# Performance work log

Hardware: AMD Instinct MI355X
Metric: run time of the kernel (lower is better)

Reference implementation:

```python
import jax, jax.numpy as jnp
import numpy as np

FP8_E4M3_MAX = 448.0  # torch.finfo(torch.float8_e4m3fn).max
TOKENS, D_IN, D_OUT = 8192, 4096, 4096


def setup_inputs() -> dict:
    key = jax.random.key(0)
    kx, kw, kb = jax.random.split(key, 3)
    x = jax.random.normal(kx, (TOKENS, D_IN), dtype=jnp.float32)
    # frozen bf16-like master weight, quantized to fp8 with per-tensor scale (as in __init__)
    w = jax.random.normal(kw, (D_OUT, D_IN), dtype=jnp.float32) * 0.02
    amax = jnp.abs(w).max()
    weight_scale = jnp.maximum(amax / FP8_E4M3_MAX, 1e-12).reshape(1)
    weight_fp8 = (w / weight_scale).astype(jnp.float8_e4m3fn)
    bias = jax.random.normal(kb, (D_OUT,), dtype=jnp.float32) * 0.01
    return {"x": x, "weight_fp8": weight_fp8, "weight_scale": weight_scale, "bias": bias}


def reference(x, weight_fp8, weight_scale, bias):
    # dequantize fp8 weight to activation dtype, scalar per-tensor scale
    w = weight_fp8.astype(x.dtype) * weight_scale.astype(x.dtype)  # [D_OUT, D_IN]
    return x @ w.T + bias  # [TOKENS, D_OUT]
```

## Files before the change

### kernel.cpp

```cpp
#include <hip/hip_runtime.h>


#define TILE 128
#define BKK  64
#define BK32 32
#define BM256 256
#define BN256 256

typedef __attribute__((ext_vector_type(8))) __bf16 bfrag8;
typedef __attribute__((ext_vector_type(4))) float  f32x4;
typedef __attribute__((ext_vector_type(8))) short  s8v;

#define GLOBAL_AS(p) ((const __attribute__((address_space(1))) void*)(p))
#define LDS_AS(p)    ((__attribute__((address_space(3))) void*)(p))

__device__ inline unsigned short f2bf(float f) {
    union { float f; unsigned u; } v; v.f = f;
    unsigned r = v.u + 0x7FFFu + ((v.u >> 16) & 1u);
    return (unsigned short)(r >> 16);
}
__device__ inline float bf2f(unsigned short u) {
    union { unsigned u; float f; } v; v.u = ((unsigned)u) << 16;
    return v.f;
}

__device__ inline int detect_w_f32(const void* w) {
    const unsigned short* u = (const unsigned short*)w;
    unsigned nz = 0;
#pragma unroll
    for (int i = 0; i < 64; ++i) nz |= u[2 * i];
    return nz == 0 ? 1 : 0;
}

__global__ void FP8FL_cvt_x(const float* __restrict__ x, short* __restrict__ xb, long n) {
    long i = ((long)blockIdx.x * blockDim.x + threadIdx.x) * 8;
    if (i >= n) return;
    float4 a = *(const float4*)(x + i);
    float4 b = *(const float4*)(x + i + 4);
    s8v r;
    r[0] = (short)f2bf(a.x); r[1] = (short)f2bf(a.y);
    r[2] = (short)f2bf(a.z); r[3] = (short)f2bf(a.w);
    r[4] = (short)f2bf(b.x); r[5] = (short)f2bf(b.y);
    r[6] = (short)f2bf(b.z); r[7] = (short)f2bf(b.w);
    *(s8v*)(xb + i) = r;
}

__global__ void FP8FL_cvt_w(const void* __restrict__ w, short* __restrict__ wb,
                            const float* __restrict__ scale_p, long n) {
    __shared__ int sdt;
    if (threadIdx.x == 0) sdt = detect_w_f32(w);
    __syncthreads();
    long i = ((long)blockIdx.x * blockDim.x + threadIdx.x) * 8;
    if (i >= n) return;
    const float s = scale_p[0];
    s8v r;
    if (sdt) {
        const float* wf = (const float*)w;
        float4 a = *(const float4*)(wf + i);
        float4 b = *(const float4*)(wf + i + 4);
        r[0] = (short)f2bf(a.x * s); r[1] = (short)f2bf(a.y * s);
        r[2] = (short)f2bf(a.z * s); r[3] = (short)f2bf(a.w * s);
        r[4] = (short)f2bf(b.x * s); r[5] = (short)f2bf(b.y * s);
        r[6] = (short)f2bf(b.z * s); r[7] = (short)f2bf(b.w * s);
    } else {
        const unsigned short* wu = (const unsigned short*)w;
        s8v v = *(const s8v*)(wu + i);
#pragma unroll
        for (int j = 0; j < 8; ++j)
            r[j] = (short)f2bf(bf2f((unsigned short)v[j]) * s);
    }
    *(s8v*)(wb + i) = r;
}

__device__ inline void stage_tile3(const short* __restrict__ A, const short* __restrict__ B,
                                   long row0, long col0, int K, int kc,
                                   char* __restrict__ lds, int s, int wid, int lane) {
    char* Asl = lds + s * 32768;
    char* Bsl = Asl + 16384;
#pragma unroll
    for (int i = 0; i < 2; ++i) {
        int pc = i * 512 + wid * 64 + lane;
        int r  = pc >> 2;
        int j  = (pc & 3) ^ ((r >> 1) & 3);
        const short* ga = A + (size_t)(row0 + r) * K + kc + j * 8;
        const short* gb = B + (size_t)(col0 + r) * K + kc + j * 8;
        char* da = Asl + (i * 512 + wid * 64) * 16;
        char* db = Bsl + (i * 512 + wid * 64) * 16;
        __builtin_amdgcn_global_load_lds(GLOBAL_AS(ga), LDS_AS(da), 16, 0, 0);
        __builtin_amdgcn_global_load_lds(GLOBAL_AS(gb), LDS_AS(db), 16, 0, 0);
    }
}

__global__ __launch_bounds__(512, 2)
void FP8FL_gemm256(const short* __restrict__ A, const short* __restrict__ B,
                   const float* __restrict__ bias, float* __restrict__ C,
                   int M, int N, int K) {
    __shared__ char lds[3 * 32768];

    const int tid  = threadIdx.x;
    const int lane = tid & 63;
    const int wid  = tid >> 6;

    const int nwg = gridDim.x;
    const int bid = blockIdx.x;
    const int wg  = (nwg % 8 == 0) ? (bid % 8) * (nwg / 8) + (bid / 8) : bid;

    const int tiles_n = N / BN256;
    const long row0 = (long)(wg / tiles_n) * BM256;
    const long col0 = (long)(wg % tiles_n) * BN256;

    const int wm = wid >> 2, wn = wid & 3;
    const int rl = lane & 15, g = lane >> 4;

    f32x4 acc[8][4];
#pragma unroll
    for (int m = 0; m < 8; ++m)
#pragma unroll
        for (int n = 0; n < 4; ++n) acc[m][n] = (f32x4){0.f, 0.f, 0.f, 0.f};

    const int NT = K / BK32;

    stage_tile3(A, B, row0, col0, K, 0,    lds, 0, wid, lane);
    stage_tile3(A, B, row0, col0, K, BK32, lds, 1, wid, lane);
    asm volatile("s_waitcnt vmcnt(4)" ::: "memory");
    __builtin_amdgcn_s_barrier();
    __builtin_amdgcn_sched_barrier(0);

    int scur = 0, snxt = 2;
    for (int t = 0; t < NT; ++t) {
        if (t + 2 < NT)
            stage_tile3(A, B, row0, col0, K, (t + 2) * BK32, lds, snxt, wid, lane);

        const char* Asl = lds + scur * 32768;
        const char* Bsl = Asl + 16384;
        bfrag8 af[8], bf[4];
#pragma unroll
        for (int m = 0; m < 8; ++m) {
            int r  = wm * 128 + m * 16 + rl;
            int sl = g ^ ((r >> 1) & 3);
            af[m] = *(const bfrag8*)(Asl + (r * 4 + sl) * 16);
        }
#pragma unroll
        for (int n = 0; n < 4; ++n) {
            int r  = wn * 64 + n * 16 + rl;
            int sl = g ^ ((r >> 1) & 3);
            bf[n] = *(const bfrag8*)(Bsl + (r * 4 + sl) * 16);
        }

        __builtin_amdgcn_s_setprio(1);
#pragma unroll
        for (int m = 0; m < 8; ++m)
#pragma unroll
            for (int n = 0; n < 4; ++n)
                acc[m][n] = __builtin_amdgcn_mfma_f32_16x16x32_bf16(af[m], bf[n], acc[m][n], 0, 0, 0);
        __builtin_amdgcn_s_setprio(0);

        if (t + 2 < NT) asm volatile("s_waitcnt vmcnt(4)" ::: "memory");
        else            asm volatile("s_waitcnt vmcnt(0)" ::: "memory");
        __builtin_amdgcn_s_barrier();
        __builtin_amdgcn_sched_barrier(0);

        scur = (scur == 2) ? 0 : scur + 1;
        snxt = (snxt == 2) ? 0 : snxt + 1;
    }

    float bv[4];
#pragma unroll
    for (int n = 0; n < 4; ++n) bv[n] = bias[col0 + wn * 64 + n * 16 + rl];
#pragma unroll
    for (int m = 0; m < 8; ++m) {
#pragma unroll
        for (int jj = 0; jj < 4; ++jj) {
            long r = row0 + wm * 128 + m * 16 + g * 4 + jj;
            float* cp = C + r * (long)N + col0 + wn * 64 + rl;
#pragma unroll
            for (int n = 0; n < 4; ++n) cp[n * 16] = acc[m][n][jj] + bv[n];
        }
    }
}

__global__ void FP8FL_gemm(const short* __restrict__ A, const short* __restrict__ B,
                           const float* __restrict__ bias, float* __restrict__ C,
                           int M, int N, int K) {
    __shared__ short As[TILE * BKK];
    __shared__ short Bs[TILE * BKK];

    const int tid  = threadIdx.x;
    const int lane = tid & 63;
    const int wid  = tid >> 6;

    const int nwg = gridDim.x;
    const int bid = blockIdx.x;
    const int wg  = (nwg % 8 == 0) ? (bid % 8) * (nwg / 8) + (bid / 8) : bid;

    const int tiles_n = N / TILE;
    const long row0 = (long)(wg / tiles_n) * TILE;
    const long col0 = (long)(wg % tiles_n) * TILE;

    const int wm = wid >> 1, wn = wid & 1;

    f32x4 acc[4][4];
#pragma unroll
    for (int i = 0; i < 4; ++i)
#pragma unroll
        for (int j = 0; j < 4; ++j) acc[i][j] = (f32x4){0.f, 0.f, 0.f, 0.f};

    const int rl = lane & 15;
    const int g  = lane >> 4;

    for (int k0 = 0; k0 < K; k0 += BKK) {
        __syncthreads();
#pragma unroll
        for (int i = 0; i < 4; ++i) {
            int c  = i * 256 + tid;
            int r  = c >> 3;
            int ls = c & 7;
            const short* ga = A + ((size_t)(row0 + r) * K + k0 + ls * 8);
            const short* gb = B + ((size_t)(col0 + r) * K + k0 + ls * 8);
            int ldsoff = (i * 256 + wid * 64) * 16;
            __builtin_amdgcn_global_load_lds(GLOBAL_AS(ga), LDS_AS((char*)As + ldsoff), 16, 0, 0);
            __builtin_amdgcn_global_load_lds(GLOBAL_AS(gb), LDS_AS((char*)Bs + ldsoff), 16, 0, 0);
        }
        __syncthreads();

#pragma unroll
        for (int kk = 0; kk < 2; ++kk) {
            bfrag8 af[4], bfr[4];
            const int lsk = kk * 4 + g;
#pragma unroll
            for (int m = 0; m < 4; ++m) {
                int r  = wm * 64 + m * 16 + rl;
                af[m] = *(const bfrag8*)&As[r * 64 + lsk * 8];
            }
#pragma unroll
            for (int n = 0; n < 4; ++n) {
                int r  = wn * 64 + n * 16 + rl;
                bfr[n] = *(const bfrag8*)&Bs[r * 64 + lsk * 8];
            }
#pragma unroll
            for (int m = 0; m < 4; ++m)
#pragma unroll
                for (int n = 0; n < 4; ++n)
                    acc[m][n] = __builtin_amdgcn_mfma_f32_16x16x32_bf16(af[m], bfr[n], acc[m][n], 0, 0, 0);
        }
    }

    float bv[4];
#pragma unroll
    for (int n = 0; n < 4; ++n) bv[n] = bias[col0 + wn * 64 + n * 16 + rl];
#pragma unroll
    for (int m = 0; m < 4; ++m) {
#pragma unroll
        for (int j = 0; j < 4; ++j) {
            long r = row0 + wm * 64 + m * 16 + g * 4 + j;
            float* cp = C + r * (long)N + col0 + wn * 64 + rl;
#pragma unroll
            for (int n = 0; n < 4; ++n) cp[n * 16] = acc[m][n][j] + bv[n];
        }
    }
}

__global__ void FP8FL_gemm_fused(const float* __restrict__ X, const void* __restrict__ W,
                                 const float* __restrict__ scale_p,
                                 const float* __restrict__ bias, float* __restrict__ C,
                                 int M, int N, int K) {
    __shared__ short As[TILE * BKK];
    __shared__ short Bs[TILE * BKK];
    __shared__ int sdt;

    const int tid  = threadIdx.x;
    const int lane = tid & 63;
    const int wid  = tid >> 6;

    if (tid == 0) sdt = detect_w_f32(W);
    __syncthreads();
    const int wdt = sdt;
    const float s = scale_p[0];

    const int nwg = gridDim.x;
    const int bid = blockIdx.x;
    const int wg  = (nwg % 8 == 0) ? (bid % 8) * (nwg / 8) + (bid / 8) : bid;

    const int tiles_n = N / TILE;
    const long row0 = (long)(wg / tiles_n) * TILE;
    const long col0 = (long)(wg % tiles_n) * TILE;

    const int wm = wid >> 1, wn = wid & 1;

    f32x4 acc[4][4];
#pragma unroll
    for (int i = 0; i < 4; ++i)
#pragma unroll
        for (int j = 0; j < 4; ++j) acc[i][j] = (f32x4){0.f, 0.f, 0.f, 0.f};

    const int rl = lane & 15;
    const int g  = lane >> 4;

    for (int k0 = 0; k0 < K; k0 += BKK) {
        s8v va[4], vb[4];
#pragma unroll
        for (int i = 0; i < 4; ++i) {
            int c  = i * 256 + tid;
            int r  = c >> 3;
            int ls = c & 7;
            {
                const float* xp = X + ((size_t)(row0 + r) * K + k0 + ls * 8);
                float4 a = *(const float4*)xp;
                float4 b = *(const float4*)(xp + 4);
                s8v t;
                t[0] = (short)f2bf(a.x); t[1] = (short)f2bf(a.y);
                t[2] = (short)f2bf(a.z); t[3] = (short)f2bf(a.w);
                t[4] = (short)f2bf(b.x); t[5] = (short)f2bf(b.y);
                t[6] = (short)f2bf(b.z); t[7] = (short)f2bf(b.w);
                va[i] = t;
            }
            {
                size_t off = (size_t)(col0 + r) * K + k0 + ls * 8;
                s8v t;
                if (wdt) {
                    const float* wp = (const float*)W + off;
                    float4 a = *(const float4*)wp;
                    float4 b = *(const float4*)(wp + 4);
                    t[0] = (short)f2bf(a.x * s); t[1] = (short)f2bf(a.y * s);
                    t[2] = (short)f2bf(a.z * s); t[3] = (short)f2bf(a.w * s);
                    t[4] = (short)f2bf(b.x * s); t[5] = (short)f2bf(b.y * s);
                    t[6] = (short)f2bf(b.z * s); t[7] = (short)f2bf(b.w * s);
                } else {
                    const unsigned short* wp = (const unsigned short*)W + off;
                    s8v v = *(const s8v*)wp;
#pragma unroll
                    for (int j = 0; j < 8; ++j)
                        t[j] = (short)f2bf(bf2f((unsigned short)v[j]) * s);
                }
                vb[i] = t;
            }
        }
        __syncthreads();
#pragma unroll
        for (int i = 0; i < 4; ++i) {
            int c = i * 256 + tid;
            *(s8v*)((char*)As + (size_t)c * 16) = va[i];
            *(s8v*)((char*)Bs + (size_t)c * 16) = vb[i];
        }
        __syncthreads();

#pragma unroll
        for (int kk = 0; kk < 2; ++kk) {
            bfrag8 af[4], bfr[4];
            const int lsk = kk * 4 + g;
#pragma unroll
            for (int m = 0; m < 4; ++m) {
                int r  = wm * 64 + m * 16 + rl;
                af[m] = *(const bfrag8*)&As[r * 64 + lsk * 8];
            }
#pragma unroll
            for (int n = 0; n < 4; ++n) {
                int r  = wn * 64 + n * 16 + rl;
                bfr[n] = *(const bfrag8*)&Bs[r * 64 + lsk * 8];
            }
#pragma unroll
            for (int m = 0; m < 4; ++m)
#pragma unroll
                for (int n = 0; n < 4; ++n)
                    acc[m][n] = __builtin_amdgcn_mfma_f32_16x16x32_bf16(af[m], bfr[n], acc[m][n], 0, 0, 0);
        }
    }

    float bv[4];
#pragma unroll
    for (int n = 0; n < 4; ++n) bv[n] = bias[col0 + wn * 64 + n * 16 + rl];
#pragma unroll
    for (int m = 0; m < 4; ++m) {
#pragma unroll
        for (int j = 0; j < 4; ++j) {
            long r = row0 + wm * 64 + m * 16 + g * 4 + j;
            float* cp = C + r * (long)N + col0 + wn * 64 + rl;
#pragma unroll
            for (int n = 0; n < 4; ++n) cp[n * 16] = acc[m][n][j] + bv[n];
        }
    }
}

__global__ void FP8FL_naive(const float* __restrict__ x, const void* __restrict__ w,
                            const float* __restrict__ scale_p, const float* __restrict__ bias,
                            float* __restrict__ out, int M, int N, int K) {
    __shared__ int sdt;
    if (threadIdx.x == 0) sdt = detect_w_f32(w);
    __syncthreads();
    long o = (long)blockIdx.x * blockDim.x + threadIdx.x;
    if (o >= (long)M * N) return;
    int m = (int)(o / N), n = (int)(o % N);
    const float* xr = x + (size_t)m * K;
    float acc = 0.f;
    if (sdt) {
        const float* wr = (const float*)w + (size_t)n * K;
        for (int k = 0; k < K; ++k) acc += xr[k] * wr[k];
    } else {
        const unsigned short* wr = (const unsigned short*)w + (size_t)n * K;
        for (int k = 0; k < K; ++k) acc += xr[k] * bf2f(wr[k]);
    }
    out[o] = acc * scale_p[0] + bias[n];
}

extern "C" void kernel_launch(void* const* d_in, const int* in_sizes, int n_in,
                              void* d_out, int out_size, void* d_ws, size_t ws_size,
                              hipStream_t stream) {
    const float* x     = (const float*)d_in[0];
    const void*  w     = d_in[1];
    const float* scale = (const float*)d_in[2];
    const float* bias  = (const float*)d_in[3];
    float*       out   = (float*)d_out;

    const int N = in_sizes[3];
    const int K = in_sizes[1] / N;
    const int M = in_sizes[0] / K;

    const size_t need = (size_t)M * K * 2 + (size_t)N * K * 2;
    const bool ws_ok   = ws_size >= need;
    const bool dims256 = (M % BM256 == 0) && (N % BN256 == 0) && (K % BKK == 0) && (K / BK32 >= 4);
    const bool dims128 = (M % TILE == 0) && (N % TILE == 0) && (K % BKK == 0);

    if (ws_ok && (dims256 || dims128)) {
        short* xb = (short*)d_ws;
        short* wb = (short*)((char*)d_ws + (size_t)M * K * 2);
        long nx = (long)M * K;
        long nw = (long)N * K;
        FP8FL_cvt_x<<<(int)((nx / 8 + 255) / 256), 256, 0, stream>>>(x, xb, nx);
        FP8FL_cvt_w<<<(int)((nw / 8 + 255) / 256), 256, 0, stream>>>(w, wb, scale, nw);
        if (dims256) {
            int grid = (M / BM256) * (N / BN256);
            FP8FL_gemm256<<<grid, 512, 0, stream>>>(xb, wb, bias, out, M, N, K);
        } else {
            int grid = (M / TILE) * (N / TILE);
            FP8FL_gemm<<<grid, 256, 0, stream>>>(xb, wb, bias, out, M, N, K);
        }
    } else if (dims128) {
        int grid = (M / TILE) * (N / TILE);
        FP8FL_gemm_fused<<<grid, 256, 0, stream>>>(x, w, scale, bias, out, M, N, K);
    } else {
        long total = (long)M * N;
        FP8FL_naive<<<(int)((total + 255) / 256), 256, 0, stream>>>(x, w, scale, bias, out, M, N, K);
    }
}
```

Measured before the change: 291.5 us.

## Split GEMM K-step into two half phases interleaving LDS reads, prefetch and MFMA

Each K iteration is split into two halves. Each half loads its A fragments from LDS, issues half of the next tile's global-to-LDS prefetch, then runs 16 MFMAs, with extra barriers between the phases. The aim is to spread global load issue across the compute and cut register pressure by holding only half the A fragments at a time. In exchange it adds several workgroup barriers per iteration, which can add synchronisation stalls.

```diff
diff --git a/kernel.cpp b/kernel.cpp
--- a/kernel.cpp
+++ b/kernel.cpp
@@ -72,20 +72,22 @@
     *(s8v*)(wb + i) = r;
 }
 
-__device__ inline void stage_tile3(const short* __restrict__ A, const short* __restrict__ B,
+__device__ inline void stage_half3(const short* __restrict__ A, const short* __restrict__ B,
                                    long row0, long col0, int K, int kc,
-                                   char* __restrict__ lds, int s, int wid, int lane) {
+                                   char* __restrict__ lds, int s, int h,
+                                   int wid, int lane) {
     char* Asl = lds + s * 32768;
     char* Bsl = Asl + 16384;
 #pragma unroll
-    for (int i = 0; i < 2; ++i) {
-        int pc = i * 512 + wid * 64 + lane;
+    for (int i = 0; i < 1; ++i) {}
+    {
+        int pc = (h ? 512 : 0) + wid * 64 + lane;
         int r  = pc >> 2;
         int j  = (pc & 3) ^ ((r >> 1) & 3);
         const short* ga = A + (size_t)(row0 + r) * K + kc + j * 8;
         const short* gb = B + (size_t)(col0 + r) * K + kc + j * 8;
-        char* da = Asl + (i * 512 + wid * 64) * 16;
-        char* db = Bsl + (i * 512 + wid * 64) * 16;
+        char* da = Asl + ((h ? 512 : 0) + wid * 64) * 16;
+        char* db = Bsl + ((h ? 512 : 0) + wid * 64) * 16;
         __builtin_amdgcn_global_load_lds(GLOBAL_AS(ga), LDS_AS(da), 16, 0, 0);
         __builtin_amdgcn_global_load_lds(GLOBAL_AS(gb), LDS_AS(db), 16, 0, 0);
     }
@@ -120,25 +122,27 @@
 
     const int NT = K / BK32;
 
-    stage_tile3(A, B, row0, col0, K, 0,    lds, 0, wid, lane);
-    stage_tile3(A, B, row0, col0, K, BK32, lds, 1, wid, lane);
+    stage_half3(A, B, row0, col0, K, 0,    lds, 0, 0, wid, lane);
+    stage_half3(A, B, row0, col0, K, 0,    lds, 0, 1, wid, lane);
+    stage_half3(A, B, row0, col0, K, BK32, lds, 1, 0, wid, lane);
+    stage_half3(A, B, row0, col0, K, BK32, lds, 1, 1, wid, lane);
     asm volatile("s_waitcnt vmcnt(4)" ::: "memory");
     __builtin_amdgcn_s_barrier();
     __builtin_amdgcn_sched_barrier(0);
 
     int scur = 0, snxt = 2;
     for (int t = 0; t < NT; ++t) {
-        if (t + 2 < NT)
-            stage_tile3(A, B, row0, col0, K, (t + 2) * BK32, lds, snxt, wid, lane);
-
         const char* Asl = lds + scur * 32768;
         const char* Bsl = Asl + 16384;
-        bfrag8 af[8], bf[4];
-#pragma unroll
-        for (int m = 0; m < 8; ++m) {
+        const bool pf = (t + 2 < NT);
+        const int  kc2 = (t + 2) * BK32;
+
+        bfrag8 a0[4], bf[4], a1[4];
+#pragma unroll
+        for (int m = 0; m < 4; ++m) {
             int r  = wm * 128 + m * 16 + rl;
             int sl = g ^ ((r >> 1) & 3);
-            af[m] = *(const bfrag8*)(Asl + (r * 4 + sl) * 16);
+            a0[m] = *(const bfrag8*)(Asl + (r * 4 + sl) * 16);
         }
 #pragma unroll
         for (int n = 0; n < 4; ++n) {
@@ -146,17 +150,42 @@
             int sl = g ^ ((r >> 1) & 3);
             bf[n] = *(const bfrag8*)(Bsl + (r * 4 + sl) * 16);
         }
-
+        if (pf) stage_half3(A, B, row0, col0, K, kc2, lds, snxt, 0, wid, lane);
+
+        __builtin_amdgcn_s_barrier();
+        asm volatile("s_waitcnt lgkmcnt(0)" ::: "memory");
+        __builtin_amdgcn_sched_barrier(0);
         __builtin_amdgcn_s_setprio(1);
 #pragma unroll
-        for (int m = 0; m < 8; ++m)
+        for (int m = 0; m < 4; ++m)
 #pragma unroll
             for (int n = 0; n < 4; ++n)
-                acc[m][n] = __builtin_amdgcn_mfma_f32_16x16x32_bf16(af[m], bf[n], acc[m][n], 0, 0, 0);
+                acc[m][n] = __builtin_amdgcn_mfma_f32_16x16x32_bf16(a0[m], bf[n], acc[m][n], 0, 0, 0);
         __builtin_amdgcn_s_setprio(0);
-
-        if (t + 2 < NT) asm volatile("s_waitcnt vmcnt(4)" ::: "memory");
-        else            asm volatile("s_waitcnt vmcnt(0)" ::: "memory");
+        __builtin_amdgcn_s_barrier();
+        __builtin_amdgcn_sched_barrier(0);
+
+#pragma unroll
+        for (int m = 0; m < 4; ++m) {
+            int r  = wm * 128 + (m + 4) * 16 + rl;
+            int sl = g ^ ((r >> 1) & 3);
+            a1[m] = *(const bfrag8*)(Asl + (r * 4 + sl) * 16);
+        }
+        if (pf) stage_half3(A, B, row0, col0, K, kc2, lds, snxt, 1, wid, lane);
+
+        __builtin_amdgcn_s_barrier();
+        asm volatile("s_waitcnt lgkmcnt(0)" ::: "memory");
+        __builtin_amdgcn_sched_barrier(0);
+        __builtin_amdgcn_s_setprio(1);
+#pragma unroll
+        for (int m = 0; m < 4; ++m)
+#pragma unroll
+            for (int n = 0; n < 4; ++n)
+                acc[m + 4][n] = __builtin_amdgcn_mfma_f32_16x16x32_bf16(a1[m], bf[n], acc[m + 4][n], 0, 0, 0);
+        __builtin_amdgcn_s_setprio(0);
+
+        if (pf) asm volatile("s_waitcnt vmcnt(4)" ::: "memory");
+        else    asm volatile("s_waitcnt vmcnt(0)" ::: "memory");
         __builtin_amdgcn_s_barrier();
         __builtin_amdgcn_sched_barrier(0);
 
```

Result: slower. 300.7 us (+3.1%).

## Shrink GEMM tile to 256x128 with double-buffered LDS and higher occupancy

Applied to the files above, without the earlier changes.

Replaces the 256x256 bf16 GEMM tile with a 256x128 tile, halving per-wave accumulators from 8x4 to 4x4 MFMA fragments. Launch bounds now request 4 workgroups per CU instead of 2. The LDS pipeline drops from triple buffering with explicit vmcnt waits to double buffering with plain __syncthreads. The aim is more resident waves and more tiles to spread across CUs, at the cost of less operand reuse per tile and more global traffic for A. The simpler synchronisation may also expose load latency that the earlier three-stage pipeline hid.

```diff
diff --git a/kernel.cpp b/kernel.cpp
--- a/kernel.cpp
+++ b/kernel.cpp
@@ -4,8 +4,8 @@
 #define TILE 128
 #define BKK  64
 #define BK32 32
-#define BM256 256
-#define BN256 256
+#define BM   256
+#define BN   128
 
 typedef __attribute__((ext_vector_type(8))) __bf16 bfrag8;
 typedef __attribute__((ext_vector_type(4))) float  f32x4;
@@ -72,10 +72,10 @@
     *(s8v*)(wb + i) = r;
 }
 
-__device__ inline void stage_tile3(const short* __restrict__ A, const short* __restrict__ B,
-                                   long row0, long col0, int K, int kc,
-                                   char* __restrict__ lds, int s, int wid, int lane) {
-    char* Asl = lds + s * 32768;
+__device__ inline void stage_tile(const short* __restrict__ A, const short* __restrict__ B,
+                                  long row0, long col0, int K, int kc,
+                                  char* __restrict__ lds, int d, int wid, int lane) {
+    char* Asl = lds + d * 24576;
     char* Bsl = Asl + 16384;
 #pragma unroll
     for (int i = 0; i < 2; ++i) {
@@ -83,19 +83,24 @@
         int r  = pc >> 2;
         int j  = (pc & 3) ^ ((r >> 1) & 3);
         const short* ga = A + (size_t)(row0 + r) * K + kc + j * 8;
+        char* da = Asl + (i * 512 + wid * 64) * 16;
+        __builtin_amdgcn_global_load_lds(GLOBAL_AS(ga), LDS_AS(da), 16, 0, 0);
+    }
+    {
+        int pc = wid * 64 + lane;
+        int r  = pc >> 2;
+        int j  = (pc & 3) ^ ((r >> 1) & 3);
         const short* gb = B + (size_t)(col0 + r) * K + kc + j * 8;
-        char* da = Asl + (i * 512 + wid * 64) * 16;
-        char* db = Bsl + (i * 512 + wid * 64) * 16;
-        __builtin_amdgcn_global_load_lds(GLOBAL_AS(ga), LDS_AS(da), 16, 0, 0);
+        char* db = Bsl + (wid * 64) * 16;
         __builtin_amdgcn_global_load_lds(GLOBAL_AS(gb), LDS_AS(db), 16, 0, 0);
     }
 }
 
-__global__ __launch_bounds__(512, 2)
-void FP8FL_gemm256(const short* __restrict__ A, const short* __restrict__ B,
-                   const float* __restrict__ bias, float* __restrict__ C,
-                   int M, int N, int K) {
-    __shared__ char lds[3 * 32768];
+__global__ __launch_bounds__(512, 4)
+void FP8FL_gemm256x128(const short* __restrict__ A, const short* __restrict__ B,
+                       const float* __restrict__ bias, float* __restrict__ C,
+                       int M, int N, int K) {
+    __shared__ char lds[2 * 24576];
 
     const int tid  = threadIdx.x;
     const int lane = tid & 63;
@@ -105,38 +110,35 @@
     const int bid = blockIdx.x;
     const int wg  = (nwg % 8 == 0) ? (bid % 8) * (nwg / 8) + (bid / 8) : bid;
 
-    const int tiles_n = N / BN256;
-    const long row0 = (long)(wg / tiles_n) * BM256;
-    const long col0 = (long)(wg % tiles_n) * BN256;
-
-    const int wm = wid >> 2, wn = wid & 3;
+    const int tiles_n = N / BN;
+    const long row0 = (long)(wg / tiles_n) * BM;
+    const long col0 = (long)(wg % tiles_n) * BN;
+
+    const int wm = wid >> 1, wn = wid & 1;
     const int rl = lane & 15, g = lane >> 4;
 
-    f32x4 acc[8][4];
-#pragma unroll
-    for (int m = 0; m < 8; ++m)
+    f32x4 acc[4][4];
+#pragma unroll
+    for (int m = 0; m < 4; ++m)
 #pragma unroll
         for (int n = 0; n < 4; ++n) acc[m][n] = (f32x4){0.f, 0.f, 0.f, 0.f};
 
     const int NT = K / BK32;
 
-    stage_tile3(A, B, row0, col0, K, 0,    lds, 0, wid, lane);
-    stage_tile3(A, B, row0, col0, K, BK32, lds, 1, wid, lane);
-    asm volatile("s_waitcnt vmcnt(4)" ::: "memory");
-    __builtin_amdgcn_s_barrier();
-    __builtin_amdgcn_sched_barrier(0);
-
-    int scur = 0, snxt = 2;
+    stage_tile(A, B, row0, col0, K, 0, lds, 0, wid, lane);
+    __syncthreads();
+
     for (int t = 0; t < NT; ++t) {
-        if (t + 2 < NT)
-            stage_tile3(A, B, row0, col0, K, (t + 2) * BK32, lds, snxt, wid, lane);
-
-        const char* Asl = lds + scur * 32768;
+        const int d = t & 1;
+        if (t + 1 < NT)
+            stage_tile(A, B, row0, col0, K, (t + 1) * BK32, lds, d ^ 1, wid, lane);
+
+        const char* Asl = lds + d * 24576;
         const char* Bsl = Asl + 16384;
-        bfrag8 af[8], bf[4];
-#pragma unroll
-        for (int m = 0; m < 8; ++m) {
-            int r  = wm * 128 + m * 16 + rl;
+        bfrag8 af[4], bf[4];
+#pragma unroll
+        for (int m = 0; m < 4; ++m) {
+            int r  = wm * 64 + m * 16 + rl;
             int sl = g ^ ((r >> 1) & 3);
             af[m] = *(const bfrag8*)(Asl + (r * 4 + sl) * 16);
         }
@@ -149,29 +151,23 @@
 
         __builtin_amdgcn_s_setprio(1);
 #pragma unroll
-        for (int m = 0; m < 8; ++m)
+        for (int m = 0; m < 4; ++m)
 #pragma unroll
             for (int n = 0; n < 4; ++n)
                 acc[m][n] = __builtin_amdgcn_mfma_f32_16x16x32_bf16(af[m], bf[n], acc[m][n], 0, 0, 0);
         __builtin_amdgcn_s_setprio(0);
 
-        if (t + 2 < NT) asm volatile("s_waitcnt vmcnt(4)" ::: "memory");
-        else            asm volatile("s_waitcnt vmcnt(0)" ::: "memory");
-        __builtin_amdgcn_s_barrier();
-        __builtin_amdgcn_sched_barrier(0);
-
-        scur = (scur == 2) ? 0 : scur + 1;
-        snxt = (snxt == 2) ? 0 : snxt + 1;
+        __syncthreads();
     }
 
     float bv[4];
 #pragma unroll
     for (int n = 0; n < 4; ++n) bv[n] = bias[col0 + wn * 64 + n * 16 + rl];
 #pragma unroll
-    for (int m = 0; m < 8; ++m) {
+    for (int m = 0; m < 4; ++m) {
 #pragma unroll
         for (int jj = 0; jj < 4; ++jj) {
-            long r = row0 + wm * 128 + m * 16 + g * 4 + jj;
+            long r = row0 + wm * 64 + m * 16 + g * 4 + jj;
             float* cp = C + r * (long)N + col0 + wn * 64 + rl;
 #pragma unroll
             for (int n = 0; n < 4; ++n) cp[n * 16] = acc[m][n][jj] + bv[n];
@@ -417,19 +413,19 @@
 
     const size_t need = (size_t)M * K * 2 + (size_t)N * K * 2;
     const bool ws_ok   = ws_size >= need;
-    const bool dims256 = (M % BM256 == 0) && (N % BN256 == 0) && (K % BKK == 0) && (K / BK32 >= 4);
+    const bool dimsBig = (M % BM == 0) && (N % BN == 0) && (K % BK32 == 0) && (K / BK32 >= 2);
     const bool dims128 = (M % TILE == 0) && (N % TILE == 0) && (K % BKK == 0);
 
-    if (ws_ok && (dims256 || dims128)) {
+    if (ws_ok && (dimsBig || dims128)) {
         short* xb = (short*)d_ws;
         short* wb = (short*)((char*)d_ws + (size_t)M * K * 2);
         long nx = (long)M * K;
         long nw = (long)N * K;
         FP8FL_cvt_x<<<(int)((nx / 8 + 255) / 256), 256, 0, stream>>>(x, xb, nx);
         FP8FL_cvt_w<<<(int)((nw / 8 + 255) / 256), 256, 0, stream>>>(w, wb, scale, nw);
-        if (dims256) {
-            int grid = (M / BM256) * (N / BN256);
-            FP8FL_gemm256<<<grid, 512, 0, stream>>>(xb, wb, bias, out, M, N, K);
+        if (dimsBig) {
+            int grid = (M / BM) * (N / BN);
+            FP8FL_gemm256x128<<<grid, 512, 0, stream>>>(xb, wb, bias, out, M, N, K);
         } else {
             int grid = (M / TILE) * (N / TILE);
             FP8FL_gemm<<<grid, 256, 0, stream>>>(xb, wb, bias, out, M, N, K);
```

After: 317.2 us. 8.8% more time.

## Deepen LDS ring to four stages and prefetch next A fragments into registers

Applied to the files above, without the earlier changes.

The bf16 GEMM main loop moves from a 3-slot to a 4-slot LDS ring, prefetching three K-tiles ahead. It is unrolled by two so the A fragments for the next tile are read from LDS into a second register buffer while the current tile's MFMAs run. The goal is to hide global-load latency and LDS read latency behind MFMA work. In exchange it uses 128 KB of LDS per block instead of 96 KB and needs more VGPRs for the extra fragment buffer. The sched_barrier calls that constrained instruction scheduling are also removed.

```diff
diff --git a/kernel.cpp b/kernel.cpp
--- a/kernel.cpp
+++ b/kernel.cpp
@@ -72,7 +72,7 @@
     *(s8v*)(wb + i) = r;
 }
 
-__device__ inline void stage_tile3(const short* __restrict__ A, const short* __restrict__ B,
+__device__ inline void stage_tile4(const short* __restrict__ A, const short* __restrict__ B,
                                    long row0, long col0, int K, int kc,
                                    char* __restrict__ lds, int s, int wid, int lane) {
     char* Asl = lds + s * 32768;
@@ -91,11 +91,43 @@
     }
 }
 
+#define RD_A(dst, sbase)                                                    \
+    {                                                                       \
+        _Pragma("unroll")                                                   \
+        for (int m = 0; m < 8; ++m) {                                       \
+            int r  = wm * 128 + m * 16 + rl;                                \
+            int sl = g ^ ((r >> 1) & 3);                                    \
+            dst[m] = *(const bfrag8*)((sbase) + (r * 4 + sl) * 16);         \
+        }                                                                   \
+    }
+
+#define RD_B(dst, sbase)                                                    \
+    {                                                                       \
+        _Pragma("unroll")                                                   \
+        for (int n = 0; n < 4; ++n) {                                       \
+            int r  = wn * 64 + n * 16 + rl;                                 \
+            int sl = g ^ ((r >> 1) & 3);                                    \
+            dst[n] = *(const bfrag8*)((sbase) + 16384 + (r * 4 + sl) * 16); \
+        }                                                                   \
+    }
+
+#define MM(fa, bb)                                                          \
+    {                                                                       \
+        __builtin_amdgcn_s_setprio(1);                                      \
+        _Pragma("unroll")                                                   \
+        for (int m = 0; m < 8; ++m)                                         \
+            _Pragma("unroll")                                               \
+            for (int n = 0; n < 4; ++n)                                     \
+                acc[m][n] = __builtin_amdgcn_mfma_f32_16x16x32_bf16(        \
+                    fa[m], bb[n], acc[m][n], 0, 0, 0);                      \
+        __builtin_amdgcn_s_setprio(0);                                      \
+    }
+
 __global__ __launch_bounds__(512, 2)
 void FP8FL_gemm256(const short* __restrict__ A, const short* __restrict__ B,
                    const float* __restrict__ bias, float* __restrict__ C,
                    int M, int N, int K) {
-    __shared__ char lds[3 * 32768];
+    __shared__ char lds[4 * 32768];
 
     const int tid  = threadIdx.x;
     const int lane = tid & 63;
@@ -120,48 +152,34 @@
 
     const int NT = K / BK32;
 
-    stage_tile3(A, B, row0, col0, K, 0,    lds, 0, wid, lane);
-    stage_tile3(A, B, row0, col0, K, BK32, lds, 1, wid, lane);
+    stage_tile4(A, B, row0, col0, K, 0,        lds, 0, wid, lane);
+    stage_tile4(A, B, row0, col0, K, BK32,     lds, 1, wid, lane);
+    stage_tile4(A, B, row0, col0, K, 2 * BK32, lds, 2, wid, lane);
     asm volatile("s_waitcnt vmcnt(4)" ::: "memory");
     __builtin_amdgcn_s_barrier();
-    __builtin_amdgcn_sched_barrier(0);
-
-    int scur = 0, snxt = 2;
-    for (int t = 0; t < NT; ++t) {
-        if (t + 2 < NT)
-            stage_tile3(A, B, row0, col0, K, (t + 2) * BK32, lds, snxt, wid, lane);
-
-        const char* Asl = lds + scur * 32768;
-        const char* Bsl = Asl + 16384;
-        bfrag8 af[8], bf[4];
-#pragma unroll
-        for (int m = 0; m < 8; ++m) {
-            int r  = wm * 128 + m * 16 + rl;
-            int sl = g ^ ((r >> 1) & 3);
-            af[m] = *(const bfrag8*)(Asl + (r * 4 + sl) * 16);
-        }
-#pragma unroll
-        for (int n = 0; n < 4; ++n) {
-            int r  = wn * 64 + n * 16 + rl;
-            int sl = g ^ ((r >> 1) & 3);
-            bf[n] = *(const bfrag8*)(Bsl + (r * 4 + sl) * 16);
-        }
-
-        __builtin_amdgcn_s_setprio(1);
-#pragma unroll
-        for (int m = 0; m < 8; ++m)
-#pragma unroll
-            for (int n = 0; n < 4; ++n)
-                acc[m][n] = __builtin_amdgcn_mfma_f32_16x16x32_bf16(af[m], bf[n], acc[m][n], 0, 0, 0);
-        __builtin_amdgcn_s_setprio(0);
-
-        if (t + 2 < NT) asm volatile("s_waitcnt vmcnt(4)" ::: "memory");
+
+    bfrag8 FA[8], FB[8], BB[4];
+    RD_A(FA, lds);
+
+    for (int t = 0; t < NT; t += 2) {
+        if (t + 3 < NT)
+            stage_tile4(A, B, row0, col0, K, (t + 3) * BK32, lds, (t + 3) & 3, wid, lane);
+        RD_A(FB, lds + ((t + 1) & 3) * 32768);
+        RD_B(BB, lds + (t & 3) * 32768);
+        MM(FA, BB);
+        if (t + 3 < NT) asm volatile("s_waitcnt vmcnt(4)" ::: "memory");
         else            asm volatile("s_waitcnt vmcnt(0)" ::: "memory");
         __builtin_amdgcn_s_barrier();
-        __builtin_amdgcn_sched_barrier(0);
-
-        scur = (scur == 2) ? 0 : scur + 1;
-        snxt = (snxt == 2) ? 0 : snxt + 1;
+
+        if (t + 4 < NT)
+            stage_tile4(A, B, row0, col0, K, (t + 4) * BK32, lds, (t + 4) & 3, wid, lane);
+        if (t + 2 < NT)
+            RD_A(FA, lds + ((t + 2) & 3) * 32768);
+        RD_B(BB, lds + ((t + 1) & 3) * 32768);
+        MM(FB, BB);
+        if (t + 4 < NT) asm volatile("s_waitcnt vmcnt(4)" ::: "memory");
+        else            asm volatile("s_waitcnt vmcnt(0)" ::: "memory");
+        __builtin_amdgcn_s_barrier();
     }
 
     float bv[4];
```

Result: no change. 292.1 us (+0.2%).
